# Kernel tuning notes

Measured on AMD Instinct MI355X. Metric: run time of the kernel, lower is better.

## Reference

```python
import jax, jax.numpy as jnp
import numpy as np

N_HEADS, D_MODEL, D_HEAD = 16, 1024, 64
BATCH, SEQ = 2, 2048
INIT_STD = 0.02
MASK_FILL = -100000.0  # module uses -1e5, not -inf


def setup_inputs() -> dict:
    key = jax.random.key(0)
    ks = jax.random.split(key, 5)
    x = jax.random.normal(ks[0], (BATCH, SEQ, D_MODEL), dtype=jnp.float32)
    W_Q = INIT_STD * jax.random.normal(ks[1], (N_HEADS, D_MODEL, D_HEAD), dtype=jnp.float32)
    W_K = INIT_STD * jax.random.normal(ks[2], (N_HEADS, D_MODEL, D_HEAD), dtype=jnp.float32)
    W_V = INIT_STD * jax.random.normal(ks[3], (N_HEADS, D_MODEL, D_HEAD), dtype=jnp.float32)
    W_O = INIT_STD * jax.random.normal(ks[4], (N_HEADS, D_HEAD, D_MODEL), dtype=jnp.float32)
    b_Q = jnp.zeros((N_HEADS, D_HEAD), dtype=jnp.float32)
    b_K = jnp.zeros((N_HEADS, D_HEAD), dtype=jnp.float32)
    b_V = jnp.zeros((N_HEADS, D_HEAD), dtype=jnp.float32)
    b_O = jnp.zeros((D_MODEL,), dtype=jnp.float32)
    return {"normalized_resid_pre": x, "W_Q": W_Q, "W_K": W_K, "W_V": W_V,
            "W_O": W_O, "b_Q": b_Q, "b_K": b_K, "b_V": b_V, "b_O": b_O}


def reference(normalized_resid_pre, W_Q, W_K, W_V, W_O, b_Q, b_K, b_V, b_O):
    x = normalized_resid_pre  # [b, s, d_model]
    Q = jnp.einsum('bpd,hde->bphe', x, W_Q) + b_Q  # [b, s, h, dh]
    K = jnp.einsum('bpd,hde->bphe', x, W_K) + b_K
    V = jnp.einsum('bpd,hde->bphe', x, W_V) + b_V
    scale = 1.0 / jnp.sqrt(jnp.float32(D_HEAD))
    scores = jnp.einsum('bqhe,bkhe->bhqk', Q, K) * scale  # [b, h, q, k]
    s = scores.shape[-1]
    causal = jnp.triu(jnp.ones((s, s), dtype=bool), k=1)  # True above diagonal
    scores = jnp.where(causal, jnp.float32(MASK_FILL), scores)
    attn = jax.nn.softmax(scores, axis=-1)
    Z = jnp.einsum('bkhe,bhqk->bqhe', V, attn)  # [b, q, h, dh]
    out = jnp.einsum('bqhe,hed->bqd', Z, W_O) + b_O  # [b, q, d_model]
    return out
```

## Files before the change

kernel.cpp:

```cpp
#include <hip/hip_runtime.h>
#include <math.h>

#define BATCH 2
#define SEQ   2048
#define NH    16
#define DH    64
#define DM    1024

typedef __attribute__((ext_vector_type(8))) short bf16x8;
typedef __attribute__((ext_vector_type(8))) unsigned short u16x8;
typedef __attribute__((ext_vector_type(4))) float f32x4;

__device__ __forceinline__ unsigned short f2bf(float f) {
    union { float f; unsigned u; } v; v.f = f;
    unsigned r = v.u + 0x7FFF + ((v.u >> 16) & 1);
    return (unsigned short)(r >> 16);
}
__device__ __forceinline__ unsigned short f2bf_fast(float f) {
    union { float f; unsigned u; } v; v.f = f;
    return (unsigned short)((v.u + 0x8000u) >> 16);
}

__global__ __launch_bounds__(256) void conv_fused(
    const float* __restrict__ x,
    const float* __restrict__ WQ, const float* __restrict__ WK,
    const float* __restrict__ WV, const float* __restrict__ WO,
    unsigned short* __restrict__ xb,
    unsigned short* __restrict__ Wt, unsigned short* __restrict__ WOt)
{
    __shared__ float sT[64][68];
    const int tid = threadIdx.x;

    if (blockIdx.x < 2048) {
        size_t idx = ((size_t)blockIdx.x * 256 + tid) * 8;
        float4 a = *(const float4*)(x + idx);
        float4 b = *(const float4*)(x + idx + 4);
        u16x8 o;
        o[0] = f2bf(a.x); o[1] = f2bf(a.y); o[2] = f2bf(a.z); o[3] = f2bf(a.w);
        o[4] = f2bf(b.x); o[5] = f2bf(b.y); o[6] = f2bf(b.z); o[7] = f2bf(b.w);
        *(u16x8*)(xb + idx) = o;
        return;
    }
    const int t = blockIdx.x - 2048;
    if (t < 768) {
        int m = t >> 8, rem = t & 255, h = rem >> 4, dblk = rem & 15;
        const float* W = (m == 0) ? WQ : (m == 1) ? WK : WV;
        const float* in = W + (size_t)h * 65536 + dblk * 4096;
#pragma unroll
        for (int it = 0; it < 4; it++) {
            int idx = it * 1024 + tid * 4;
            int r = idx >> 6, c = idx & 63;
            *(float4*)(&sT[r][c]) = *(const float4*)(&in[(size_t)r * 64 + c]);
        }
        __syncthreads();
        unsigned short* out = Wt + (size_t)m * 1048576 + (size_t)h * 65536 + dblk * 64;
#pragma unroll
        for (int it = 0; it < 4; it++) {
            int idx = it * 1024 + tid * 4;
            int e = idx >> 6, d0 = idx & 63;
            ushort4 o;
            unsigned short* op = (unsigned short*)&o;
#pragma unroll
            for (int j = 0; j < 4; j++) op[j] = f2bf(sT[d0 + j][e]);
            *(ushort4*)&out[(size_t)e * 1024 + d0] = o;
        }
    } else {
        int tt = t - 768, rblk = tt >> 4, cblk = tt & 15;
        const float* in = WO + (size_t)rblk * 64 * 1024 + cblk * 64;
#pragma unroll
        for (int it = 0; it < 4; it++) {
            int idx = it * 1024 + tid * 4;
            int r = idx >> 6, c = idx & 63;
            *(float4*)(&sT[r][c]) = *(const float4*)(&in[(size_t)r * 1024 + c]);
        }
        __syncthreads();
        unsigned short* out = WOt + (size_t)cblk * 64 * 1024 + rblk * 64;
#pragma unroll
        for (int it = 0; it < 4; it++) {
            int idx = it * 1024 + tid * 4;
            int d = idx >> 6, he0 = idx & 63;
            ushort4 o;
            unsigned short* op = (unsigned short*)&o;
#pragma unroll
            for (int j = 0; j < 4; j++) op[j] = f2bf(sT[he0 + j][d]);
            *(ushort4*)&out[(size_t)d * 1024 + he0] = o;
        }
    }
}

__global__ __launch_bounds__(256) void qkv_mfma(
    const unsigned short* __restrict__ xb,
    const unsigned short* __restrict__ Wt,
    const float* __restrict__ bQ, const float* __restrict__ bK,
    const float* __restrict__ bV,
    unsigned short* __restrict__ Q, unsigned short* __restrict__ K,
    unsigned short* __restrict__ Vt)
{
    __shared__ __align__(16) unsigned short sA[2][128 * 40];
    __shared__ __align__(16) unsigned short sB[2][128 * 40];

    const int rowTile = blockIdx.x;
    const int m  = blockIdx.y >> 3;
    const int hp = blockIdx.y & 7;
    const unsigned short* Wm = Wt + (size_t)m * 1048576 + (size_t)hp * 2 * 65536;

    const int tid  = threadIdx.x;
    const int w    = tid >> 6;
    const int lane = tid & 63;
    const int l15  = lane & 15;
    const int quad = lane >> 4;
    const int rw   = (w & 1) * 64;
    const int cw   = (w >> 1) * 64;
    const int rowBase = rowTile * 128;

    f32x4 acc[4][4];
#pragma unroll
    for (int i = 0; i < 4; i++)
#pragma unroll
        for (int j = 0; j < 4; j++) acc[i][j] = (f32x4){0.f, 0.f, 0.f, 0.f};

    const int sr = tid >> 2;
    const int sc = (tid & 3) * 8;

    u16x8 rA0 = *(const u16x8*)&xb[(size_t)(rowBase + sr) * DM + sc];
    u16x8 rA1 = *(const u16x8*)&xb[(size_t)(rowBase + sr + 64) * DM + sc];
    u16x8 rB0 = *(const u16x8*)&Wm[(size_t)sr * DM + sc];
    u16x8 rB1 = *(const u16x8*)&Wm[(size_t)(sr + 64) * DM + sc];

    for (int kt = 0; kt < 32; kt++) {
        const int p = kt & 1;
        unsigned short* pA = sA[p];
        unsigned short* pB = sB[p];
        *(u16x8*)&pA[sr * 40 + sc]        = rA0;
        *(u16x8*)&pA[(sr + 64) * 40 + sc] = rA1;
        *(u16x8*)&pB[sr * 40 + sc]        = rB0;
        *(u16x8*)&pB[(sr + 64) * 40 + sc] = rB1;
        __syncthreads();

        if (kt < 31) {
            const int k1 = (kt + 1) * 32;
            rA0 = *(const u16x8*)&xb[(size_t)(rowBase + sr) * DM + k1 + sc];
            rA1 = *(const u16x8*)&xb[(size_t)(rowBase + sr + 64) * DM + k1 + sc];
            rB0 = *(const u16x8*)&Wm[(size_t)sr * DM + k1 + sc];
            rB1 = *(const u16x8*)&Wm[(size_t)(sr + 64) * DM + k1 + sc];
        }

        bf16x8 af[4], bf[4];
#pragma unroll
        for (int i = 0; i < 4; i++)
            af[i] = *(const bf16x8*)&pA[(rw + i * 16 + l15) * 40 + quad * 8];
#pragma unroll
        for (int j = 0; j < 4; j++)
            bf[j] = *(const bf16x8*)&pB[(cw + j * 16 + l15) * 40 + quad * 8];
        if (m == 2) {
#pragma unroll
            for (int i = 0; i < 4; i++)
#pragma unroll
                for (int j = 0; j < 4; j++)
                    acc[i][j] = __builtin_amdgcn_mfma_f32_16x16x32_bf16(
                        af[i], bf[j], acc[i][j], 0, 0, 0);
        } else {
#pragma unroll
            for (int i = 0; i < 4; i++)
#pragma unroll
                for (int j = 0; j < 4; j++)
                    acc[i][j] = __builtin_amdgcn_mfma_f32_16x16x32_bf16(
                        bf[j], af[i], acc[i][j], 0, 0, 0);
        }
    }

    if (m == 2) {
#pragma unroll
        for (int j = 0; j < 4; j++) {
            int col = cw + j * 16 + l15;
            int h = hp * 2 + (col >> 6);
            int e = col & 63;
            float bv = bV[h * DH + e];
#pragma unroll
            for (int i = 0; i < 4; i++) {
                int row0 = rowBase + rw + i * 16 + quad * 4;
                int b = row0 >> 11, s0 = row0 & 2047;
                ushort4 o;
                unsigned short* op = (unsigned short*)&o;
#pragma unroll
                for (int r = 0; r < 4; r++) op[r] = f2bf(acc[i][j][r] + bv);
                *(ushort4*)&Vt[(((size_t)b * NH + h) * DH + e) * SEQ + s0] = o;
            }
        }
    } else {
        const float* bias = (m == 0) ? bQ : bK;
        unsigned short* Out = (m == 0) ? Q : K;
        const float scale = (m == 0) ? 0.125f : 1.0f;
#pragma unroll
        for (int i = 0; i < 4; i++) {
            int row = rowBase + rw + i * 16 + l15;
            int b = row >> 11, s = row & 2047;
#pragma unroll
            for (int j = 0; j < 4; j++) {
                int col0 = cw + j * 16 + quad * 4;
                int h = hp * 2 + (col0 >> 6);
                int e0 = col0 & 63;
                ushort4 o;
                unsigned short* op = (unsigned short*)&o;
#pragma unroll
                for (int r = 0; r < 4; r++)
                    op[r] = f2bf((acc[i][j][r] + bias[h * DH + e0 + r]) * scale);
                *(ushort4*)&Out[(((size_t)b * NH + h) * SEQ + s) * DH + e0] = o;
            }
        }
    }
}

__global__ __launch_bounds__(256) void attn_mfma(
    const unsigned short* __restrict__ Q,
    const unsigned short* __restrict__ K,
    const unsigned short* __restrict__ Vt,
    unsigned short* __restrict__ Z)
{
    __shared__ __align__(16) unsigned short sK[2][64 * 72];
    __shared__ __align__(16) unsigned short sV[2][64 * 72];
    __shared__ __align__(16) unsigned short sPA[64 * 72];
    __shared__ __align__(16) unsigned short sPB[64 * 72];

    const int h   = blockIdx.x & 15;
    const int b   = (blockIdx.x >> 4) & 1;
    const int i   = blockIdx.x >> 5;
    const int qtA = i;
    const int qtB = 31 - i;

    const int tid  = threadIdx.x;
    const int w    = tid >> 6;
    const int lane = tid & 63;
    const int l15  = lane & 15;
    const int quad = lane >> 4;

    const size_t headOff = ((size_t)b * NH + h) * SEQ * DH;
    const unsigned short* Qh  = Q  + headOff;
    const unsigned short* Kh  = K  + headOff;
    const unsigned short* Vth = Vt + headOff;

    const unsigned short* qrowA =
        Qh + (size_t)(qtA * 64 + w * 16 + l15) * DH + quad * 8;
    const unsigned short* qrowB =
        Qh + (size_t)(qtB * 64 + w * 16 + l15) * DH + quad * 8;
    bf16x8 qA[2], qB[2];
    qA[0] = *(const bf16x8*)(qrowA);  qA[1] = *(const bf16x8*)(qrowA + 32);
    qB[0] = *(const bf16x8*)(qrowB);  qB[1] = *(const bf16x8*)(qrowB + 32);

    f32x4 OA[4], OB[4];
#pragma unroll
    for (int s = 0; s < 4; s++) {
        OA[s] = (f32x4){0.f, 0.f, 0.f, 0.f};
        OB[s] = (f32x4){0.f, 0.f, 0.f, 0.f};
    }
    float lAa = 0.f, lBa = 0.f;

    const int r0 = tid >> 3;
    const int c0 = (tid & 7) * 8;

    u16x8 rK0 = *(const u16x8*)&Kh[(size_t)r0 * DH + c0];
    u16x8 rK1 = *(const u16x8*)&Kh[(size_t)(r0 + 32) * DH + c0];
    u16x8 rV0 = *(const u16x8*)&Vth[(size_t)r0 * SEQ + c0];
    u16x8 rV1 = *(const u16x8*)&Vth[(size_t)(r0 + 32) * SEQ + c0];

    for (int kt = 0; kt <= qtB; kt++) {
        const int p = kt & 1;
        unsigned short* bKp = sK[p];
        unsigned short* bVp = sV[p];
        *(u16x8*)&bKp[r0 * 72 + c0]        = rK0;
        *(u16x8*)&bKp[(r0 + 32) * 72 + c0] = rK1;
        *(u16x8*)&bVp[r0 * 72 + c0]        = rV0;
        *(u16x8*)&bVp[(r0 + 32) * 72 + c0] = rV1;
        __syncthreads();

        if (kt < qtB) {
            const int k1 = (kt + 1) * 64;
            rK0 = *(const u16x8*)&Kh[(size_t)(k1 + r0) * DH + c0];
            rK1 = *(const u16x8*)&Kh[(size_t)(k1 + r0 + 32) * DH + c0];
            rV0 = *(const u16x8*)&Vth[(size_t)r0 * SEQ + k1 + c0];
            rV1 = *(const u16x8*)&Vth[(size_t)(r0 + 32) * SEQ + k1 + c0];
        }

        bf16x8 kf[8], vf[8];
#pragma unroll
        for (int ks = 0; ks < 2; ks++)
#pragma unroll
            for (int sub = 0; sub < 4; sub++) {
                kf[ks * 4 + sub] = *(const bf16x8*)
                    &bKp[(sub * 16 + l15) * 72 + ks * 32 + quad * 8];
                vf[ks * 4 + sub] = *(const bf16x8*)
                    &bVp[(sub * 16 + l15) * 72 + ks * 32 + quad * 8];
            }

        const bool doA = (kt <= qtA);

        f32x4 SB[4];
#pragma unroll
        for (int s = 0; s < 4; s++) SB[s] = (f32x4){0.f, 0.f, 0.f, 0.f};
#pragma unroll
        for (int ks = 0; ks < 2; ks++)
#pragma unroll
            for (int sub = 0; sub < 4; sub++)
                SB[sub] = __builtin_amdgcn_mfma_f32_16x16x32_bf16(
                    kf[ks * 4 + sub], qB[ks], SB[sub], 0, 0, 0);
        f32x4 SA[4];
        if (doA) {
#pragma unroll
            for (int s = 0; s < 4; s++) SA[s] = (f32x4){0.f, 0.f, 0.f, 0.f};
#pragma unroll
            for (int ks = 0; ks < 2; ks++)
#pragma unroll
                for (int sub = 0; sub < 4; sub++)
                    SA[sub] = __builtin_amdgcn_mfma_f32_16x16x32_bf16(
                        kf[ks * 4 + sub], qA[ks], SA[sub], 0, 0, 0);
        }

        const bool diagB = (kt == qtB);
#pragma unroll
        for (int sub = 0; sub < 4; sub++) {
            ushort4 o;
            unsigned short* op = (unsigned short*)&o;
#pragma unroll
            for (int r = 0; r < 4; r++) {
                float pb = __expf(SB[sub][r]);
                if (diagB && (sub * 16 + quad * 4 + r > w * 16 + l15)) pb = 0.f;
                lBa += pb;
                op[r] = f2bf_fast(pb);
            }
            *(ushort4*)&sPB[(w * 16 + l15) * 72 + sub * 16 + quad * 4] = o;
        }
        if (doA) {
            const bool diagA = (kt == qtA);
#pragma unroll
            for (int sub = 0; sub < 4; sub++) {
                ushort4 o;
                unsigned short* op = (unsigned short*)&o;
#pragma unroll
                for (int r = 0; r < 4; r++) {
                    float pa = __expf(SA[sub][r]);
                    if (diagA && (sub * 16 + quad * 4 + r > w * 16 + l15)) pa = 0.f;
                    lAa += pa;
                    op[r] = f2bf_fast(pa);
                }
                *(ushort4*)&sPA[(w * 16 + l15) * 72 + sub * 16 + quad * 4] = o;
            }
        }
        __builtin_amdgcn_wave_barrier();

#pragma unroll
        for (int ks = 0; ks < 2; ks++) {
            bf16x8 pb = *(const bf16x8*)
                &sPB[(w * 16 + l15) * 72 + ks * 32 + quad * 8];
#pragma unroll
            for (int sub = 0; sub < 4; sub++)
                OB[sub] = __builtin_amdgcn_mfma_f32_16x16x32_bf16(
                    vf[ks * 4 + sub], pb, OB[sub], 0, 0, 0);
        }
        if (doA) {
#pragma unroll
            for (int ks = 0; ks < 2; ks++) {
                bf16x8 pa = *(const bf16x8*)
                    &sPA[(w * 16 + l15) * 72 + ks * 32 + quad * 8];
#pragma unroll
                for (int sub = 0; sub < 4; sub++)
                    OA[sub] = __builtin_amdgcn_mfma_f32_16x16x32_bf16(
                        vf[ks * 4 + sub], pa, OA[sub], 0, 0, 0);
            }
        }
        __builtin_amdgcn_wave_barrier();
    }

    lAa += __shfl_xor(lAa, 16, 64);
    lAa += __shfl_xor(lAa, 32, 64);
    lBa += __shfl_xor(lBa, 16, 64);
    lBa += __shfl_xor(lBa, 32, 64);
    const float rlA = 1.0f / lAa;
    const float rlB = 1.0f / lBa;

#pragma unroll
    for (int half = 0; half < 2; half++) {
        const int qt = half ? qtB : qtA;
        const f32x4* O4 = half ? OB : OA;
        const float rl = half ? rlB : rlA;
        const int q = qt * 64 + w * 16 + l15;
        unsigned short* zrow = Z + ((size_t)b * SEQ + q) * DM + h * DH;
#pragma unroll
        for (int sub = 0; sub < 4; sub++) {
            ushort4 o;
            unsigned short* op = (unsigned short*)&o;
#pragma unroll
            for (int r = 0; r < 4; r++) op[r] = f2bf(O4[sub][r] * rl);
            *(ushort4*)&zrow[sub * 16 + quad * 4] = o;
        }
    }
}

__global__ __launch_bounds__(256) void out_mfma(
    const unsigned short* __restrict__ Zb,
    const unsigned short* __restrict__ WOt,
    const float* __restrict__ bO,
    float* __restrict__ out)
{
    __shared__ __align__(16) unsigned short sA[2][64 * 40];
    __shared__ __align__(16) unsigned short sB[2][128 * 40];

    const int rowTile = blockIdx.x;
    const int colTile = blockIdx.y;
    const int rowBase = rowTile * 64;
    const int colBase = colTile * 128;

    const int tid  = threadIdx.x;
    const int w    = tid >> 6;
    const int lane = tid & 63;
    const int l15  = lane & 15;
    const int quad = lane >> 4;
    const int rw   = (w & 1) * 32;
    const int cw   = (w >> 1) * 64;

    f32x4 acc[2][4];
#pragma unroll
    for (int i = 0; i < 2; i++)
#pragma unroll
        for (int j = 0; j < 4; j++) acc[i][j] = (f32x4){0.f, 0.f, 0.f, 0.f};

    const int sr = tid >> 2;
    const int sc = (tid & 3) * 8;

    u16x8 rA0 = *(const u16x8*)&Zb[(size_t)(rowBase + sr) * DM + sc];
    u16x8 rB0 = *(const u16x8*)&WOt[(size_t)(colBase + sr) * DM + sc];
    u16x8 rB1 = *(const u16x8*)&WOt[(size_t)(colBase + sr + 64) * DM + sc];

    for (int kt = 0; kt < 32; kt++) {
        const int p = kt & 1;
        unsigned short* pA = sA[p];
        unsigned short* pB = sB[p];
        *(u16x8*)&pA[sr * 40 + sc]        = rA0;
        *(u16x8*)&pB[sr * 40 + sc]        = rB0;
        *(u16x8*)&pB[(sr + 64) * 40 + sc] = rB1;
        __syncthreads();

        if (kt < 31) {
            const int k1 = (kt + 1) * 32;
            rA0 = *(const u16x8*)&Zb[(size_t)(rowBase + sr) * DM + k1 + sc];
            rB0 = *(const u16x8*)&WOt[(size_t)(colBase + sr) * DM + k1 + sc];
            rB1 = *(const u16x8*)&WOt[(size_t)(colBase + sr + 64) * DM + k1 + sc];
        }

        bf16x8 af[2], bf[4];
#pragma unroll
        for (int i = 0; i < 2; i++)
            af[i] = *(const bf16x8*)&pA[(rw + i * 16 + l15) * 40 + quad * 8];
#pragma unroll
        for (int j = 0; j < 4; j++)
            bf[j] = *(const bf16x8*)&pB[(cw + j * 16 + l15) * 40 + quad * 8];
#pragma unroll
        for (int i = 0; i < 2; i++)
#pragma unroll
            for (int j = 0; j < 4; j++)
                acc[i][j] = __builtin_amdgcn_mfma_f32_16x16x32_bf16(
                    bf[j], af[i], acc[i][j], 0, 0, 0);
    }

#pragma unroll
    for (int i = 0; i < 2; i++) {
        int row = rowBase + rw + i * 16 + l15;
#pragma unroll
        for (int j = 0; j < 4; j++) {
            int col0 = colBase + cw + j * 16 + quad * 4;
            float4 o;
            o.x = acc[i][j][0] + bO[col0 + 0];
            o.y = acc[i][j][1] + bO[col0 + 1];
            o.z = acc[i][j][2] + bO[col0 + 2];
            o.w = acc[i][j][3] + bO[col0 + 3];
            *(float4*)&out[(size_t)row * DM + col0] = o;
        }
    }
}

extern "C" void kernel_launch(void* const* d_in, const int* in_sizes, int n_in,
                              void* d_out, int out_size, void* d_ws, size_t ws_size,
                              hipStream_t stream)
{
    const float* x  = (const float*)d_in[0];
    const float* WQ = (const float*)d_in[1];
    const float* WK = (const float*)d_in[2];
    const float* WV = (const float*)d_in[3];
    const float* WO = (const float*)d_in[4];
    const float* bQ = (const float*)d_in[5];
    const float* bK = (const float*)d_in[6];
    const float* bV = (const float*)d_in[7];
    const float* bO = (const float*)d_in[8];
    float* out = (float*)d_out;

    const size_t M4 = 4194304;
    unsigned short* xb  = (unsigned short*)d_ws;
    unsigned short* Wt  = xb + M4;
    unsigned short* WOt = Wt + 3 * 1048576;
    unsigned short* Qw  = WOt + 1048576;
    unsigned short* Kw  = Qw + M4;
    unsigned short* Vtw = Kw + M4;
    unsigned short* Zb  = xb;

    conv_fused<<<3072, 256, 0, stream>>>(x, WQ, WK, WV, WO, xb, Wt, WOt);

    dim3 g1(32, 24);
    qkv_mfma<<<g1, 256, 0, stream>>>(xb, Wt, bQ, bK, bV, Qw, Kw, Vtw);

    attn_mfma<<<512, 256, 0, stream>>>(Qw, Kw, Vtw, Zb);

    dim3 g3(64, 8);
    out_mfma<<<g3, 256, 0, stream>>>(Zb, WOt, bO, out);
}
```

Before: 217.8 us.

## Load GEMM and attention tiles directly into LDS with XOR-swizzled layout

Replaces the register-staged, double-buffered global-to-shared copies in the QKV, attention and output kernels with direct global_load_lds 16-byte transfers into single-buffered LDS tiles. The tiles use an XOR swizzle instead of padding to avoid bank conflicts, and the GEMM K-step grows from 32 to 64. This removes register staging and the LDS store instructions, but drops the software prefetch overlap: each iteration now waits on its load between two barriers, which risks exposing global memory latency.

```diff
diff --git a/kernel.cpp b/kernel.cpp
--- a/kernel.cpp
+++ b/kernel.cpp
@@ -19,6 +19,13 @@
 __device__ __forceinline__ unsigned short f2bf_fast(float f) {
     union { float f; unsigned u; } v; v.f = f;
     return (unsigned short)((v.u + 0x8000u) >> 16);
+}
+
+__device__ __forceinline__ void gl2lds16(const void* g, void* l) {
+    __builtin_amdgcn_global_load_lds(
+        (const __attribute__((address_space(1))) void*)g,
+        (__attribute__((address_space(3))) void*)l,
+        16, 0, 0);
 }
 
 __global__ __launch_bounds__(256) void conv_fused(
@@ -96,8 +103,8 @@
     unsigned short* __restrict__ Q, unsigned short* __restrict__ K,
     unsigned short* __restrict__ Vt)
 {
-    __shared__ __align__(16) unsigned short sA[2][128 * 40];
-    __shared__ __align__(16) unsigned short sB[2][128 * 40];
+    __shared__ __align__(16) unsigned short sA[128 * 64];
+    __shared__ __align__(16) unsigned short sB[128 * 64];
 
     const int rowTile = blockIdx.x;
     const int m  = blockIdx.y >> 3;
@@ -113,59 +120,54 @@
     const int cw   = (w >> 1) * 64;
     const int rowBase = rowTile * 128;
 
+    const int crow = lane >> 3;
+    const int ccs  = (((lane & 7) ^ crow) * 8);
+
     f32x4 acc[4][4];
 #pragma unroll
     for (int i = 0; i < 4; i++)
 #pragma unroll
         for (int j = 0; j < 4; j++) acc[i][j] = (f32x4){0.f, 0.f, 0.f, 0.f};
 
-    const int sr = tid >> 2;
-    const int sc = (tid & 3) * 8;
-
-    u16x8 rA0 = *(const u16x8*)&xb[(size_t)(rowBase + sr) * DM + sc];
-    u16x8 rA1 = *(const u16x8*)&xb[(size_t)(rowBase + sr + 64) * DM + sc];
-    u16x8 rB0 = *(const u16x8*)&Wm[(size_t)sr * DM + sc];
-    u16x8 rB1 = *(const u16x8*)&Wm[(size_t)(sr + 64) * DM + sc];
-
-    for (int kt = 0; kt < 32; kt++) {
-        const int p = kt & 1;
-        unsigned short* pA = sA[p];
-        unsigned short* pB = sB[p];
-        *(u16x8*)&pA[sr * 40 + sc]        = rA0;
-        *(u16x8*)&pA[(sr + 64) * 40 + sc] = rA1;
-        *(u16x8*)&pB[sr * 40 + sc]        = rB0;
-        *(u16x8*)&pB[(sr + 64) * 40 + sc] = rB1;
-        __syncthreads();
-
-        if (kt < 31) {
-            const int k1 = (kt + 1) * 32;
-            rA0 = *(const u16x8*)&xb[(size_t)(rowBase + sr) * DM + k1 + sc];
-            rA1 = *(const u16x8*)&xb[(size_t)(rowBase + sr + 64) * DM + k1 + sc];
-            rB0 = *(const u16x8*)&Wm[(size_t)sr * DM + k1 + sc];
-            rB1 = *(const u16x8*)&Wm[(size_t)(sr + 64) * DM + k1 + sc];
-        }
-
-        bf16x8 af[4], bf[4];
-#pragma unroll
-        for (int i = 0; i < 4; i++)
-            af[i] = *(const bf16x8*)&pA[(rw + i * 16 + l15) * 40 + quad * 8];
-#pragma unroll
-        for (int j = 0; j < 4; j++)
-            bf[j] = *(const bf16x8*)&pB[(cw + j * 16 + l15) * 40 + quad * 8];
-        if (m == 2) {
-#pragma unroll
-            for (int i = 0; i < 4; i++)
-#pragma unroll
-                for (int j = 0; j < 4; j++)
-                    acc[i][j] = __builtin_amdgcn_mfma_f32_16x16x32_bf16(
-                        af[i], bf[j], acc[i][j], 0, 0, 0);
-        } else {
-#pragma unroll
-            for (int i = 0; i < 4; i++)
-#pragma unroll
-                for (int j = 0; j < 4; j++)
-                    acc[i][j] = __builtin_amdgcn_mfma_f32_16x16x32_bf16(
-                        bf[j], af[i], acc[i][j], 0, 0, 0);
+    for (int k0 = 0; k0 < DM; k0 += 64) {
+        __syncthreads();
+#pragma unroll
+        for (int c = 0; c < 4; c++) {
+            const int chunk = w * 4 + c;
+            const int rr = chunk * 8 + crow;
+            gl2lds16(&xb[(size_t)(rowBase + rr) * DM + k0 + ccs], &sA[chunk * 512]);
+            gl2lds16(&Wm[(size_t)rr * DM + k0 + ccs],             &sB[chunk * 512]);
+        }
+        __syncthreads();
+
+#pragma unroll
+        for (int ks = 0; ks < 2; ks++) {
+            bf16x8 af[4], bf[4];
+#pragma unroll
+            for (int i = 0; i < 4; i++) {
+                int ar = rw + i * 16 + l15;
+                af[i] = *(const bf16x8*)&sA[ar * 64 + (((ks * 4 + quad) ^ (ar & 7)) * 8)];
+            }
+#pragma unroll
+            for (int j = 0; j < 4; j++) {
+                int br = cw + j * 16 + l15;
+                bf[j] = *(const bf16x8*)&sB[br * 64 + (((ks * 4 + quad) ^ (br & 7)) * 8)];
+            }
+            if (m == 2) {
+#pragma unroll
+                for (int i = 0; i < 4; i++)
+#pragma unroll
+                    for (int j = 0; j < 4; j++)
+                        acc[i][j] = __builtin_amdgcn_mfma_f32_16x16x32_bf16(
+                            af[i], bf[j], acc[i][j], 0, 0, 0);
+            } else {
+#pragma unroll
+                for (int i = 0; i < 4; i++)
+#pragma unroll
+                    for (int j = 0; j < 4; j++)
+                        acc[i][j] = __builtin_amdgcn_mfma_f32_16x16x32_bf16(
+                            bf[j], af[i], acc[i][j], 0, 0, 0);
+            }
         }
     }
 
@@ -217,8 +219,8 @@
     const unsigned short* __restrict__ Vt,
     unsigned short* __restrict__ Z)
 {
-    __shared__ __align__(16) unsigned short sK[2][64 * 72];
-    __shared__ __align__(16) unsigned short sV[2][64 * 72];
+    __shared__ __align__(16) unsigned short sK [64 * 64];
+    __shared__ __align__(16) unsigned short sV [64 * 64];
     __shared__ __align__(16) unsigned short sPA[64 * 72];
     __shared__ __align__(16) unsigned short sPB[64 * 72];
 
@@ -255,41 +257,30 @@
     }
     float lAa = 0.f, lBa = 0.f;
 
-    const int r0 = tid >> 3;
-    const int c0 = (tid & 7) * 8;
-
-    u16x8 rK0 = *(const u16x8*)&Kh[(size_t)r0 * DH + c0];
-    u16x8 rK1 = *(const u16x8*)&Kh[(size_t)(r0 + 32) * DH + c0];
-    u16x8 rV0 = *(const u16x8*)&Vth[(size_t)r0 * SEQ + c0];
-    u16x8 rV1 = *(const u16x8*)&Vth[(size_t)(r0 + 32) * SEQ + c0];
+    const int crow = lane >> 3;
+    const int ccs  = (((lane & 7) ^ crow) * 8);
 
     for (int kt = 0; kt <= qtB; kt++) {
-        const int p = kt & 1;
-        unsigned short* bKp = sK[p];
-        unsigned short* bVp = sV[p];
-        *(u16x8*)&bKp[r0 * 72 + c0]        = rK0;
-        *(u16x8*)&bKp[(r0 + 32) * 72 + c0] = rK1;
-        *(u16x8*)&bVp[r0 * 72 + c0]        = rV0;
-        *(u16x8*)&bVp[(r0 + 32) * 72 + c0] = rV1;
-        __syncthreads();
-
-        if (kt < qtB) {
-            const int k1 = (kt + 1) * 64;
-            rK0 = *(const u16x8*)&Kh[(size_t)(k1 + r0) * DH + c0];
-            rK1 = *(const u16x8*)&Kh[(size_t)(k1 + r0 + 32) * DH + c0];
-            rV0 = *(const u16x8*)&Vth[(size_t)r0 * SEQ + k1 + c0];
-            rV1 = *(const u16x8*)&Vth[(size_t)(r0 + 32) * SEQ + k1 + c0];
-        }
+        const int k0 = kt * 64;
+        __syncthreads();
+#pragma unroll
+        for (int c = 0; c < 2; c++) {
+            const int chunk = w * 2 + c;
+            const int rr = chunk * 8 + crow;
+            gl2lds16(&Kh[(size_t)(k0 + rr) * DH + ccs], &sK[chunk * 512]);
+            gl2lds16(&Vth[(size_t)rr * SEQ + k0 + ccs], &sV[chunk * 512]);
+        }
+        __syncthreads();
 
         bf16x8 kf[8], vf[8];
 #pragma unroll
         for (int ks = 0; ks < 2; ks++)
 #pragma unroll
             for (int sub = 0; sub < 4; sub++) {
-                kf[ks * 4 + sub] = *(const bf16x8*)
-                    &bKp[(sub * 16 + l15) * 72 + ks * 32 + quad * 8];
-                vf[ks * 4 + sub] = *(const bf16x8*)
-                    &bVp[(sub * 16 + l15) * 72 + ks * 32 + quad * 8];
+                int rr = sub * 16 + l15;
+                int sw = ((ks * 4 + quad) ^ (rr & 7)) * 8;
+                kf[ks * 4 + sub] = *(const bf16x8*)&sK[rr * 64 + sw];
+                vf[ks * 4 + sub] = *(const bf16x8*)&sV[rr * 64 + sw];
             }
 
         const bool doA = (kt <= qtA);
@@ -401,8 +392,8 @@
     const float* __restrict__ bO,
     float* __restrict__ out)
 {
-    __shared__ __align__(16) unsigned short sA[2][64 * 40];
-    __shared__ __align__(16) unsigned short sB[2][128 * 40];
+    __shared__ __align__(16) unsigned short sA[64 * 64];
+    __shared__ __align__(16) unsigned short sB[128 * 64];
 
     const int rowTile = blockIdx.x;
     const int colTile = blockIdx.y;
@@ -417,48 +408,51 @@
     const int rw   = (w & 1) * 32;
     const int cw   = (w >> 1) * 64;
 
+    const int crow = lane >> 3;
+    const int ccs  = (((lane & 7) ^ crow) * 8);
+
     f32x4 acc[2][4];
 #pragma unroll
     for (int i = 0; i < 2; i++)
 #pragma unroll
         for (int j = 0; j < 4; j++) acc[i][j] = (f32x4){0.f, 0.f, 0.f, 0.f};
 
-    const int sr = tid >> 2;
-    const int sc = (tid & 3) * 8;
-
-    u16x8 rA0 = *(const u16x8*)&Zb[(size_t)(rowBase + sr) * DM + sc];
-    u16x8 rB0 = *(const u16x8*)&WOt[(size_t)(colBase + sr) * DM + sc];
-    u16x8 rB1 = *(const u16x8*)&WOt[(size_t)(colBase + sr + 64) * DM + sc];
-
-    for (int kt = 0; kt < 32; kt++) {
-        const int p = kt & 1;
-        unsigned short* pA = sA[p];
-        unsigned short* pB = sB[p];
-        *(u16x8*)&pA[sr * 40 + sc]        = rA0;
-        *(u16x8*)&pB[sr * 40 + sc]        = rB0;
-        *(u16x8*)&pB[(sr + 64) * 40 + sc] = rB1;
-        __syncthreads();
-
-        if (kt < 31) {
-            const int k1 = (kt + 1) * 32;
-            rA0 = *(const u16x8*)&Zb[(size_t)(rowBase + sr) * DM + k1 + sc];
-            rB0 = *(const u16x8*)&WOt[(size_t)(colBase + sr) * DM + k1 + sc];
-            rB1 = *(const u16x8*)&WOt[(size_t)(colBase + sr + 64) * DM + k1 + sc];
-        }
-
-        bf16x8 af[2], bf[4];
-#pragma unroll
-        for (int i = 0; i < 2; i++)
-            af[i] = *(const bf16x8*)&pA[(rw + i * 16 + l15) * 40 + quad * 8];
-#pragma unroll
-        for (int j = 0; j < 4; j++)
-            bf[j] = *(const bf16x8*)&pB[(cw + j * 16 + l15) * 40 + quad * 8];
-#pragma unroll
-        for (int i = 0; i < 2; i++)
-#pragma unroll
-            for (int j = 0; j < 4; j++)
-                acc[i][j] = __builtin_amdgcn_mfma_f32_16x16x32_bf16(
-                    bf[j], af[i], acc[i][j], 0, 0, 0);
+    for (int k0 = 0; k0 < DM; k0 += 64) {
+        __syncthreads();
+#pragma unroll
+        for (int c = 0; c < 2; c++) {
+            const int chunk = w * 2 + c;
+            const int rr = chunk * 8 + crow;
+            gl2lds16(&Zb[(size_t)(rowBase + rr) * DM + k0 + ccs], &sA[chunk * 512]);
+        }
+#pragma unroll
+        for (int c = 0; c < 4; c++) {
+            const int chunk = w * 4 + c;
+            const int rr = chunk * 8 + crow;
+            gl2lds16(&WOt[(size_t)(colBase + rr) * DM + k0 + ccs], &sB[chunk * 512]);
+        }
+        __syncthreads();
+
+#pragma unroll
+        for (int ks = 0; ks < 2; ks++) {
+            bf16x8 af[2], bf[4];
+#pragma unroll
+            for (int i = 0; i < 2; i++) {
+                int ar = rw + i * 16 + l15;
+                af[i] = *(const bf16x8*)&sA[ar * 64 + (((ks * 4 + quad) ^ (ar & 7)) * 8)];
+            }
+#pragma unroll
+            for (int j = 0; j < 4; j++) {
+                int br = cw + j * 16 + l15;
+                bf[j] = *(const bf16x8*)&sB[br * 64 + (((ks * 4 + quad) ^ (br & 7)) * 8)];
+            }
+#pragma unroll
+            for (int i = 0; i < 2; i++)
+#pragma unroll
+                for (int j = 0; j < 4; j++)
+                    acc[i][j] = __builtin_amdgcn_mfma_f32_16x16x32_bf16(
+                        bf[j], af[i], acc[i][j], 0, 0, 0);
+        }
     }
 
 #pragma unroll
```

Result: faster. 201.8 us (-7.3%).
